# Kernel tuning notes

Measured on AMD Instinct MI355X. Metric: run time of the kernel, lower is better.

Reference implementation:

```python
import jax, jax.numpy as jnp
import numpy as np

B, N, DIM, T, H, DH = 4, 2048, 512, 16, 8, 64
EPS = 1e-5


def setup_inputs() -> dict:
    key = jax.random.key(0)
    ks = jax.random.split(key, 7)
    x = jax.random.normal(ks[0], (B, N, DIM), dtype=jnp.float32)
    # time-distance matrix, e.g. months between scans, in [0, 24)
    R = jax.random.uniform(ks[1], (B, T, T), dtype=jnp.float32) * 24.0
    gamma = jnp.ones((DIM,), dtype=jnp.float32)
    beta = jnp.zeros((DIM,), dtype=jnp.float32)
    W_qkv = jax.random.normal(ks[2], (DIM, 3 * H * DH), dtype=jnp.float32) * 0.02
    W_out = jax.random.normal(ks[3], (H * DH, DIM), dtype=jnp.float32) * 0.02
    a = jax.random.uniform(ks[4], (H,), dtype=jnp.float32)          # torch.rand(heads)
    c = 12.0 * jax.random.uniform(ks[5], (H,), dtype=jnp.float32)   # 12 * torch.rand(heads)
    return {"x": x, "R": R, "gamma": gamma, "beta": beta,
            "W_qkv": W_qkv, "W_out": W_out, "a": a, "c": c}


def reference(x, R, gamma, beta, W_qkv, W_out, a, c):
    b, n, dim = x.shape
    t = R.shape[-1]
    num_patches = n // t
    scale = DH ** -0.5

    # LayerNorm
    mu = jnp.mean(x, axis=-1, keepdims=True)
    var = jnp.mean(jnp.square(x - mu), axis=-1, keepdims=True)
    xn = (x - mu) * jax.lax.rsqrt(var + EPS) * gamma + beta

    # QKV projection -> [b, h, n, d]
    qkv = xn @ W_qkv  # [b, n, 3*h*d]
    q, k, v = jnp.split(qkv, 3, axis=-1)
    def to_heads(z):
        return z.reshape(b, n, H, DH).transpose(0, 2, 1, 3)
    q, k, v = to_heads(q), to_heads(k), to_heads(v)

    # attention scores with ReLU then learned sigmoid time-decay mask
    dots = jnp.einsum('bhnd,bhmd->bhnm', q, k) * scale
    dots = jax.nn.relu(dots)

    # flipped-sigmoid decay: 1 / (1 + exp(|a|*R - |c|)), per head  -> [b, h, t, t]
    decay = 1.0 / (1.0 + jnp.exp(jnp.abs(a)[None, :, None, None] * R[:, None, :, :]
                                 - jnp.abs(c)[None, :, None, None]))
    # expand timepoint mask to token resolution (repeat_interleave on both axes)
    decay = jnp.repeat(jnp.repeat(decay, num_patches, axis=2), num_patches, axis=3)

    attn = jax.nn.softmax(dots * decay, axis=-1)
    out = jnp.einsum('bhnm,bhmd->bhnd', attn, v)
    out = out.transpose(0, 2, 1, 3).reshape(b, n, H * DH)
    return out @ W_out  # dropout is identity at eval
```

## Files before the change

kernel.cpp:

```cpp
#include <hip/hip_runtime.h>
#include <math.h>

#define B_   4
#define N_   2048
#define DIM_ 512
#define T_   16
#define H_   8
#define DH_  64

typedef unsigned short ushort_t;
typedef __attribute__((ext_vector_type(8))) short bf16x8;
typedef __attribute__((ext_vector_type(16))) float f32x16;

__device__ inline ushort_t bf16_rn(float x) {
  unsigned u = __builtin_bit_cast(unsigned, x);
  u += 0x7FFFu + ((u >> 16) & 1u);
  return (ushort_t)(u >> 16);
}
__device__ inline float bf16f(ushort_t h) {
  return __builtin_bit_cast(float, (unsigned)h << 16);
}
__device__ inline unsigned pack2(ushort_t a, ushort_t b) {
  return (unsigned)a | ((unsigned)b << 16);
}
__device__ inline void split2(float x, ushort_t &h, ushort_t &l) {
  h = bf16_rn(x);
  l = bf16_rn(x - bf16f(h));
}

__global__ __launch_bounds__(256) void prep_kernel(
    const float* __restrict__ x, const float* __restrict__ gamma,
    const float* __restrict__ beta, const float* __restrict__ Wqkv,
    const float* __restrict__ Wout,
    ushort_t* __restrict__ xnh, ushort_t* __restrict__ xnl,
    ushort_t* __restrict__ wqh, ushort_t* __restrict__ wql,
    ushort_t* __restrict__ woh, ushort_t* __restrict__ wol) {
  __shared__ float Ts[64][68];
  int bidx = blockIdx.x;
  int tid = threadIdx.x;
  if (bidx < 256) {
    const float* src; ushort_t* dh; ushort_t* dl; int Nn, n0, k0;
    if (bidx < 192) {
      src = Wqkv; dh = wqh; dl = wql; Nn = 1536;
      n0 = (bidx % 24) * 64; k0 = (bidx / 24) * 64;
    } else {
      int l = bidx - 192;
      src = Wout; dh = woh; dl = wol; Nn = 512;
      n0 = (l % 8) * 64; k0 = (l / 8) * 64;
    }
#pragma unroll
    for (int it = 0; it < 4; ++it) {
      int idx = tid + it * 256;
      int r = idx >> 4, c4 = (idx & 15) * 4;
      *(float4*)&Ts[r][c4] = *(const float4*)&src[(size_t)(k0 + r) * Nn + n0 + c4];
    }
    __syncthreads();
#pragma unroll
    for (int it = 0; it < 2; ++it) {
      int idx = tid + it * 256;
      int n = idx >> 3, kc = (idx & 7) * 8;
      ushort_t hs[8], ls[8];
#pragma unroll
      for (int j = 0; j < 8; ++j) split2(Ts[kc + j][n], hs[j], ls[j]);
      uint4 uh, ul;
      uh.x = pack2(hs[0], hs[1]); uh.y = pack2(hs[2], hs[3]);
      uh.z = pack2(hs[4], hs[5]); uh.w = pack2(hs[6], hs[7]);
      ul.x = pack2(ls[0], ls[1]); ul.y = pack2(ls[2], ls[3]);
      ul.z = pack2(ls[4], ls[5]); ul.w = pack2(ls[6], ls[7]);
      size_t o = (size_t)(n0 + n) * 512 + k0 + kc;
      *(uint4*)&dh[o] = uh;
      *(uint4*)&dl[o] = ul;
    }
  } else {
    int row  = (bidx - 256) * 4 + (tid >> 6);
    int lane = tid & 63;
    const float4* xr = (const float4*)(x + (size_t)row * DIM_);
    float4 v0 = xr[lane * 2 + 0];
    float4 v1 = xr[lane * 2 + 1];
    float s  = v0.x + v0.y + v0.z + v0.w + v1.x + v1.y + v1.z + v1.w;
    float ss = v0.x*v0.x + v0.y*v0.y + v0.z*v0.z + v0.w*v0.w
             + v1.x*v1.x + v1.y*v1.y + v1.z*v1.z + v1.w*v1.w;
#pragma unroll
    for (int off = 32; off > 0; off >>= 1) {
      s  += __shfl_xor(s, off);
      ss += __shfl_xor(ss, off);
    }
    float mu  = s * (1.0f / DIM_);
    float var = ss * (1.0f / DIM_) - mu * mu;
    float rstd = rsqrtf(var + 1e-5f);
    float4 g0 = *(const float4*)&gamma[lane * 8];
    float4 g1 = *(const float4*)&gamma[lane * 8 + 4];
    float4 b0 = *(const float4*)&beta[lane * 8];
    float4 b1 = *(const float4*)&beta[lane * 8 + 4];
    float xv[8] = {v0.x, v0.y, v0.z, v0.w, v1.x, v1.y, v1.z, v1.w};
    float gv[8] = {g0.x, g0.y, g0.z, g0.w, g1.x, g1.y, g1.z, g1.w};
    float bv[8] = {b0.x, b0.y, b0.z, b0.w, b1.x, b1.y, b1.z, b1.w};
    ushort_t hs[8], ls[8];
#pragma unroll
    for (int j = 0; j < 8; ++j) {
      float xn = (xv[j] - mu) * rstd * gv[j] + bv[j];
      split2(xn, hs[j], ls[j]);
    }
    uint4 uh, ul;
    uh.x = pack2(hs[0], hs[1]); uh.y = pack2(hs[2], hs[3]);
    uh.z = pack2(hs[4], hs[5]); uh.w = pack2(hs[6], hs[7]);
    ul.x = pack2(ls[0], ls[1]); ul.y = pack2(ls[2], ls[3]);
    ul.z = pack2(ls[4], ls[5]); ul.w = pack2(ls[6], ls[7]);
    size_t o = (size_t)row * DIM_ + lane * 8;
    *(uint4*)&xnh[o] = uh;
    *(uint4*)&xnl[o] = ul;
  }
}

__global__ __launch_bounds__(256) void qkv_gemm_mfma(
    const ushort_t* __restrict__ xnh, const ushort_t* __restrict__ xnl,
    const ushort_t* __restrict__ wth, const ushort_t* __restrict__ wtl,
    ushort_t* __restrict__ qh, ushort_t* __restrict__ ql,
    ushort_t* __restrict__ kho, ushort_t* __restrict__ klo,
    ushort_t* __restrict__ vt) {
  __shared__ ushort_t Ah[128 * 40], Al[128 * 40], Bh[128 * 40], Bl[128 * 40];
  int tid = threadIdx.x;
  int w = tid >> 6, lane = tid & 63, l31 = lane & 31, g = lane >> 5;
  int wm = w >> 1, wn = w & 1;
  int idx = blockIdx.x;
  int xcd = idx & 7, local = idx >> 3;
  int n0 = (local % 12) * 128;
  int m0 = ((local / 12) * 8 + xcd) * 128;

  f32x16 acc[2][2];
#pragma unroll
  for (int i = 0; i < 2; ++i)
#pragma unroll
    for (int j = 0; j < 2; ++j)
#pragma unroll
      for (int e = 0; e < 16; ++e) acc[i][j][e] = 0.0f;

  int fm[2], fc[2];
#pragma unroll
  for (int it = 0; it < 2; ++it) {
    int f = tid + it * 256;
    fm[it] = f >> 2;
    fc[it] = (f & 3) * 8;
  }

#pragma unroll 1
  for (int kt = 0; kt < 16; ++kt) {
    __syncthreads();
#pragma unroll
    for (int it = 0; it < 2; ++it) {
      size_t ao = (size_t)(m0 + fm[it]) * 512 + kt * 32 + fc[it];
      size_t bo = (size_t)(n0 + fm[it]) * 512 + kt * 32 + fc[it];
      uint4 tah = *(const uint4*)&xnh[ao];
      uint4 tal = *(const uint4*)&xnl[ao];
      uint4 tbh = *(const uint4*)&wth[bo];
      uint4 tbl = *(const uint4*)&wtl[bo];
      int o = fm[it] * 40 + fc[it];
      *(uint4*)&Ah[o] = tah;
      *(uint4*)&Al[o] = tal;
      *(uint4*)&Bh[o] = tbh;
      *(uint4*)&Bl[o] = tbl;
    }
    __syncthreads();
#pragma unroll
    for (int kc = 0; kc < 2; ++kc) {
      int off = kc * 16 + 8 * g;
      bf16x8 afh[2], afl[2], bfh[2], bfl[2];
#pragma unroll
      for (int rb = 0; rb < 2; ++rb) {
        int r = (wm * 64 + rb * 32 + l31) * 40 + off;
        afh[rb] = *(const bf16x8*)&Ah[r];
        afl[rb] = *(const bf16x8*)&Al[r];
      }
#pragma unroll
      for (int cb = 0; cb < 2; ++cb) {
        int r = (wn * 64 + cb * 32 + l31) * 40 + off;
        bfh[cb] = *(const bf16x8*)&Bh[r];
        bfl[cb] = *(const bf16x8*)&Bl[r];
      }
#pragma unroll
      for (int rb = 0; rb < 2; ++rb)
#pragma unroll
        for (int cb = 0; cb < 2; ++cb) {
          acc[rb][cb] = __builtin_amdgcn_mfma_f32_32x32x16_bf16(afh[rb], bfh[cb], acc[rb][cb], 0, 0, 0);
          acc[rb][cb] = __builtin_amdgcn_mfma_f32_32x32x16_bf16(afh[rb], bfl[cb], acc[rb][cb], 0, 0, 0);
          acc[rb][cb] = __builtin_amdgcn_mfma_f32_32x32x16_bf16(afl[rb], bfh[cb], acc[rb][cb], 0, 0, 0);
        }
    }
  }

  int part = n0 >> 9;
#pragma unroll
  for (int rb = 0; rb < 2; ++rb) {
    int m_base = m0 + wm * 64 + rb * 32;
#pragma unroll
    for (int cb = 0; cb < 2; ++cb) {
      int n_g = n0 + wn * 64 + cb * 32 + l31;
      int rem = n_g & 511, hh = rem >> 6, d = rem & 63;
      if (part == 2) {
#pragma unroll
        for (int grp = 0; grp < 4; ++grp) {
          int m_g = m_base + grp * 8 + 4 * g;
          int bb = m_g >> 11, tok = m_g & 2047;
          uint2 pk;
          pk.x = pack2(bf16_rn(acc[rb][cb][grp * 4 + 0]), bf16_rn(acc[rb][cb][grp * 4 + 1]));
          pk.y = pack2(bf16_rn(acc[rb][cb][grp * 4 + 2]), bf16_rn(acc[rb][cb][grp * 4 + 3]));
          *(uint2*)&vt[((size_t)(bb * 8 + hh) * 64 + d) * 2048 + tok] = pk;
        }
      } else {
        float sc = (part == 0) ? 0.125f : 1.0f;
        ushort_t* dsth = (part == 0) ? qh : kho;
        ushort_t* dstl = (part == 0) ? ql : klo;
#pragma unroll
        for (int reg = 0; reg < 16; ++reg) {
          int row = (reg & 3) + 8 * (reg >> 2) + 4 * g;
          int m_g = m_base + row;
          int bb = m_g >> 11, tok = m_g & 2047;
          ushort_t hi, lo;
          split2(acc[rb][cb][reg] * sc, hi, lo);
          size_t addr = ((size_t)(bb * 8 + hh) * 2048 + tok) * 64 + d;
          dsth[addr] = hi;
          dstl[addr] = lo;
        }
      }
    }
  }
}

__global__ __launch_bounds__(512) void attn_mfma(
    const ushort_t* __restrict__ qh, const ushort_t* __restrict__ ql,
    const ushort_t* __restrict__ kho, const ushort_t* __restrict__ klo,
    const ushort_t* __restrict__ vt, const float* __restrict__ R,
    const float* __restrict__ a, const float* __restrict__ c,
    ushort_t* __restrict__ aoh, ushort_t* __restrict__ aol) {
  __shared__ ushort_t KhS[64 * 72], KlS[64 * 72], VtS[64 * 72];
  __shared__ ushort_t PS[256 * 72];

  int tid = threadIdx.x;
  int w = tid >> 6, lane = tid & 63, l31 = lane & 31, g = lane >> 5;
  int bh = blockIdx.x;
  int qt = blockIdx.y;
  int b = bh >> 3, h = bh & 7;
  float aab = fabsf(a[h]);
  float cab = fabsf(c[h]);

  int qrow = qt * 256 + w * 32 + l31;
  size_t qoff = ((size_t)bh * 2048 + qrow) * 64;
  bf16x8 qfh[4], qfl[4];
#pragma unroll
  for (int d0i = 0; d0i < 4; ++d0i) {
    qfh[d0i] = *(const bf16x8*)&qh[qoff + d0i * 16 + 8 * g];
    qfl[d0i] = *(const bf16x8*)&ql[qoff + d0i * 16 + 8 * g];
  }

  int frow = tid >> 3;
  int fcc = (tid & 7) * 8;
  const ushort_t* kbase = kho + (size_t)bh * 2048 * 64;
  const ushort_t* lbase = klo + (size_t)bh * 2048 * 64;
  const ushort_t* vbase = vt + (size_t)bh * 64 * 2048;

  f32x16 oacc[2];
#pragma unroll
  for (int t = 0; t < 2; ++t)
#pragma unroll
    for (int i = 0; i < 16; ++i) oacc[t][i] = 0.0f;
  float rs_acc[16] = {};
  int ti = qt * 2 + (w >> 2);

#pragma unroll 1
  for (int kt = 0; kt < 32; ++kt) {
    __syncthreads();
    {
      uint4 tk = *(const uint4*)&kbase[(size_t)(kt * 64 + frow) * 64 + fcc];
      uint4 tl = *(const uint4*)&lbase[(size_t)(kt * 64 + frow) * 64 + fcc];
      uint4 tv = *(const uint4*)&vbase[(size_t)frow * 2048 + kt * 64 + fcc];
      int o = frow * 72 + fcc;
      *(uint4*)&KhS[o] = tk;
      *(uint4*)&KlS[o] = tl;
      *(uint4*)&VtS[o] = tv;
    }
    __syncthreads();

    float Rv = R[b * (T_ * T_) + ti * T_ + (kt >> 1)];
    float dec = 1.0f / (1.0f + __expf(aab * Rv - cab));

#pragma unroll
    for (int khalf = 0; khalf < 2; ++khalf) {
      f32x16 sacc;
#pragma unroll
      for (int i = 0; i < 16; ++i) sacc[i] = 0.0f;
      int krow = (khalf * 32 + l31) * 72;
#pragma unroll
      for (int d0i = 0; d0i < 4; ++d0i) {
        int off = krow + d0i * 16 + 8 * g;
        bf16x8 kfh = *(const bf16x8*)&KhS[off];
        bf16x8 kfl = *(const bf16x8*)&KlS[off];
        sacc = __builtin_amdgcn_mfma_f32_32x32x16_bf16(qfh[d0i], kfh, sacc, 0, 0, 0);
        sacc = __builtin_amdgcn_mfma_f32_32x32x16_bf16(qfh[d0i], kfl, sacc, 0, 0, 0);
        sacc = __builtin_amdgcn_mfma_f32_32x32x16_bf16(qfl[d0i], kfh, sacc, 0, 0, 0);
      }
#pragma unroll
      for (int reg = 0; reg < 16; ++reg) {
        float pv = __expf(fmaxf(sacc[reg], 0.0f) * dec);
        rs_acc[reg] += pv;
        int row = (reg & 3) + 8 * (reg >> 2) + 4 * g;
        PS[(w * 32 + row) * 72 + khalf * 32 + l31] = bf16_rn(pv);
      }
    }

    bf16x8 pf[4];
#pragma unroll
    for (int k0i = 0; k0i < 4; ++k0i)
      pf[k0i] = *(const bf16x8*)&PS[(w * 32 + l31) * 72 + k0i * 16 + 8 * g];
#pragma unroll
    for (int dt = 0; dt < 2; ++dt) {
      int vrow = (dt * 32 + l31) * 72;
#pragma unroll
      for (int k0i = 0; k0i < 4; ++k0i) {
        bf16x8 vf = *(const bf16x8*)&VtS[vrow + k0i * 16 + 8 * g];
        oacc[dt] = __builtin_amdgcn_mfma_f32_32x32x16_bf16(pf[k0i], vf, oacc[dt], 0, 0, 0);
      }
    }
  }

#pragma unroll
  for (int reg = 0; reg < 16; ++reg) {
    float vsum = rs_acc[reg];
    vsum += __shfl_xor(vsum, 1);
    vsum += __shfl_xor(vsum, 2);
    vsum += __shfl_xor(vsum, 4);
    vsum += __shfl_xor(vsum, 8);
    vsum += __shfl_xor(vsum, 16);
    rs_acc[reg] = vsum;
  }

#pragma unroll
  for (int reg = 0; reg < 16; ++reg) {
    int row = (reg & 3) + 8 * (reg >> 2) + 4 * g;
    float invs = 1.0f / rs_acc[reg];
    int tok = qt * 256 + w * 32 + row;
#pragma unroll
    for (int dt = 0; dt < 2; ++dt) {
      int d = dt * 32 + l31;
      ushort_t hi, lo;
      split2(oacc[dt][reg] * invs, hi, lo);
      size_t addr = ((size_t)b * 2048 + tok) * 512 + h * 64 + d;
      aoh[addr] = hi;
      aol[addr] = lo;
    }
  }
}

__global__ __launch_bounds__(256) void out_gemm_mfma(
    const ushort_t* __restrict__ ah, const ushort_t* __restrict__ al,
    const ushort_t* __restrict__ wth, const ushort_t* __restrict__ wtl,
    float* __restrict__ out) {
  __shared__ ushort_t Ah[128 * 40], Al[128 * 40], Bh[128 * 40], Bl[128 * 40];
  int tid = threadIdx.x;
  int w = tid >> 6, lane = tid & 63, l31 = lane & 31, g = lane >> 5;
  int wm = w >> 1, wn = w & 1;
  int idx = blockIdx.x;
  int xcd = idx & 7, local = idx >> 3;
  int n0 = (local & 3) * 128;
  int m0 = ((local >> 2) * 8 + xcd) * 128;

  f32x16 acc[2][2];
#pragma unroll
  for (int i = 0; i < 2; ++i)
#pragma unroll
    for (int j = 0; j < 2; ++j)
#pragma unroll
      for (int e = 0; e < 16; ++e) acc[i][j][e] = 0.0f;

  int fm[2], fc[2];
#pragma unroll
  for (int it = 0; it < 2; ++it) {
    int f = tid + it * 256;
    fm[it] = f >> 2;
    fc[it] = (f & 3) * 8;
  }

#pragma unroll 1
  for (int kt = 0; kt < 16; ++kt) {
    __syncthreads();
#pragma unroll
    for (int it = 0; it < 2; ++it) {
      size_t ao = (size_t)(m0 + fm[it]) * 512 + kt * 32 + fc[it];
      size_t bo = (size_t)(n0 + fm[it]) * 512 + kt * 32 + fc[it];
      uint4 tah = *(const uint4*)&ah[ao];
      uint4 tal = *(const uint4*)&al[ao];
      uint4 tbh = *(const uint4*)&wth[bo];
      uint4 tbl = *(const uint4*)&wtl[bo];
      int o = fm[it] * 40 + fc[it];
      *(uint4*)&Ah[o] = tah;
      *(uint4*)&Al[o] = tal;
      *(uint4*)&Bh[o] = tbh;
      *(uint4*)&Bl[o] = tbl;
    }
    __syncthreads();
#pragma unroll
    for (int kc = 0; kc < 2; ++kc) {
      int off = kc * 16 + 8 * g;
      bf16x8 afh[2], afl[2], bfh[2], bfl[2];
#pragma unroll
      for (int rb = 0; rb < 2; ++rb) {
        int r = (wm * 64 + rb * 32 + l31) * 40 + off;
        afh[rb] = *(const bf16x8*)&Ah[r];
        afl[rb] = *(const bf16x8*)&Al[r];
      }
#pragma unroll
      for (int cb = 0; cb < 2; ++cb) {
        int r = (wn * 64 + cb * 32 + l31) * 40 + off;
        bfh[cb] = *(const bf16x8*)&Bh[r];
        bfl[cb] = *(const bf16x8*)&Bl[r];
      }
#pragma unroll
      for (int rb = 0; rb < 2; ++rb)
#pragma unroll
        for (int cb = 0; cb < 2; ++cb) {
          acc[rb][cb] = __builtin_amdgcn_mfma_f32_32x32x16_bf16(afh[rb], bfh[cb], acc[rb][cb], 0, 0, 0);
          acc[rb][cb] = __builtin_amdgcn_mfma_f32_32x32x16_bf16(afh[rb], bfl[cb], acc[rb][cb], 0, 0, 0);
          acc[rb][cb] = __builtin_amdgcn_mfma_f32_32x32x16_bf16(afl[rb], bfh[cb], acc[rb][cb], 0, 0, 0);
        }
    }
  }

#pragma unroll
  for (int rb = 0; rb < 2; ++rb) {
    int m_base = m0 + wm * 64 + rb * 32;
#pragma unroll
    for (int cb = 0; cb < 2; ++cb) {
      int n_g = n0 + wn * 64 + cb * 32 + l31;
#pragma unroll
      for (int reg = 0; reg < 16; ++reg) {
        int row = (reg & 3) + 8 * (reg >> 2) + 4 * g;
        out[(size_t)(m_base + row) * 512 + n_g] = acc[rb][cb][reg];
      }
    }
  }
}

extern "C" void kernel_launch(void* const* d_in, const int* in_sizes, int n_in,
                              void* d_out, int out_size, void* d_ws, size_t ws_size,
                              hipStream_t stream) {
  (void)in_sizes; (void)n_in;
  const float* x     = (const float*)d_in[0];
  const float* R     = (const float*)d_in[1];
  const float* gamma = (const float*)d_in[2];
  const float* beta  = (const float*)d_in[3];
  const float* Wqkv  = (const float*)d_in[4];
  const float* Wout  = (const float*)d_in[5];
  const float* av    = (const float*)d_in[6];
  const float* cv    = (const float*)d_in[7];
  float* out = (float*)d_out;

  const size_t EL  = (size_t)B_ * N_ * DIM_;
  const size_t SZT = EL * sizeof(ushort_t);

  char* p = (char*)d_ws;
  ushort_t* wqh = (ushort_t*)p;                  p += (size_t)1536 * 512 * 2;
  ushort_t* wql = (ushort_t*)p;                  p += (size_t)1536 * 512 * 2;
  ushort_t* woh = (ushort_t*)p;                  p += (size_t)512 * 512 * 2;
  ushort_t* wol = (ushort_t*)p;                  p += (size_t)512 * 512 * 2;
  ushort_t* qhb = (ushort_t*)p;                  p += SZT;
  ushort_t* qlb = (ushort_t*)p;                  p += SZT;
  ushort_t* khb = (ushort_t*)p;                  p += SZT;
  ushort_t* klb = (ushort_t*)p;                  p += SZT;
  ushort_t* vtb = (ushort_t*)p;                  p += SZT;
  size_t base_need = (size_t)(p - (char*)d_ws);
  size_t needA = base_need + 2 * SZT;

  bool planA = (ws_size >= needA);
  ushort_t* xnh = planA ? (ushort_t*)p : (ushort_t*)d_out;
  ushort_t* xnl = xnh + EL;
  float* gemm_dst = planA ? out : (float*)qhb;

  prep_kernel<<<dim3(2304), dim3(256), 0, stream>>>(x, gamma, beta, Wqkv, Wout,
                                                    xnh, xnl, wqh, wql, woh, wol);
  qkv_gemm_mfma<<<dim3(768), dim3(256), 0, stream>>>(xnh, xnl, wqh, wql,
                                                     qhb, qlb, khb, klb, vtb);
  attn_mfma<<<dim3(32, 8), dim3(512), 0, stream>>>(qhb, qlb, khb, klb, vtb,
                                                   R, av, cv, xnh, xnl);
  out_gemm_mfma<<<dim3(256), dim3(256), 0, stream>>>(xnh, xnl, woh, wol, gemm_dst);
  if (!planA) {
    hipMemcpyAsync(out, gemm_dst, (size_t)out_size * sizeof(float),
                   hipMemcpyDeviceToDevice, stream);
  }
}
```

Before: 244.9 us.

## Keep attention probabilities in registers via transposed S and permlane swap

The attention kernel now computes S transposed (K as the A operand), so each lane holds one query's scores. The probabilities are packed to bf16 with v_cvt_pk_bf16_f32 and rearranged with v_permlane32_swap into the A-operand layout for the PV MFMA, which removes the shared-memory P round trip. Row sums become a per-lane scalar instead of a 5-step shuffle reduction, and exp is rewritten as exp2 with log2e folded into the decay. The block shrinks to 4 waves covering 128 query rows, with twice as many blocks, so each block reloads K/V tiles for fewer queries and global traffic rises.

Result: no change. 240.4 us (-1.8%).

```diff
diff --git a/kernel.cpp b/kernel.cpp
--- a/kernel.cpp
+++ b/kernel.cpp
@@ -26,6 +26,14 @@
 __device__ inline void split2(float x, ushort_t &h, ushort_t &l) {
   h = bf16_rn(x);
   l = bf16_rn(x - bf16f(h));
+}
+__device__ inline unsigned cvt_pk_bf16(float lo, float hi) {
+  unsigned r;
+  asm("v_cvt_pk_bf16_f32 %0, %1, %2" : "=v"(r) : "v"(lo), "v"(hi));
+  return r;
+}
+__device__ inline void permlane32_swap(unsigned &x, unsigned &y) {
+  asm volatile("v_permlane32_swap_b32 %0, %1" : "+v"(x), "+v"(y));
 }
 
 __global__ __launch_bounds__(256) void prep_kernel(
@@ -226,14 +234,14 @@
   }
 }
 
-__global__ __launch_bounds__(512) void attn_mfma(
+__global__ __launch_bounds__(256) void attn_mfma(
     const ushort_t* __restrict__ qh, const ushort_t* __restrict__ ql,
     const ushort_t* __restrict__ kho, const ushort_t* __restrict__ klo,
     const ushort_t* __restrict__ vt, const float* __restrict__ R,
     const float* __restrict__ a, const float* __restrict__ c,
     ushort_t* __restrict__ aoh, ushort_t* __restrict__ aol) {
   __shared__ ushort_t KhS[64 * 72], KlS[64 * 72], VtS[64 * 72];
-  __shared__ ushort_t PS[256 * 72];
+  __shared__ float rsS[128];
 
   int tid = threadIdx.x;
   int w = tid >> 6, lane = tid & 63, l31 = lane & 31, g = lane >> 5;
@@ -243,7 +251,7 @@
   float aab = fabsf(a[h]);
   float cab = fabsf(c[h]);
 
-  int qrow = qt * 256 + w * 32 + l31;
+  int qrow = qt * 128 + w * 32 + l31;
   size_t qoff = ((size_t)bh * 2048 + qrow) * 64;
   bf16x8 qfh[4], qfl[4];
 #pragma unroll
@@ -252,8 +260,6 @@
     qfl[d0i] = *(const bf16x8*)&ql[qoff + d0i * 16 + 8 * g];
   }
 
-  int frow = tid >> 3;
-  int fcc = (tid & 7) * 8;
   const ushort_t* kbase = kho + (size_t)bh * 2048 * 64;
   const ushort_t* lbase = klo + (size_t)bh * 2048 * 64;
   const ushort_t* vbase = vt + (size_t)bh * 64 * 2048;
@@ -263,26 +269,35 @@
   for (int t = 0; t < 2; ++t)
 #pragma unroll
     for (int i = 0; i < 16; ++i) oacc[t][i] = 0.0f;
-  float rs_acc[16] = {};
-  int ti = qt * 2 + (w >> 2);
+  float rs = 0.0f;
+
+  int frow[2], fcc[2];
+#pragma unroll
+  for (int it = 0; it < 2; ++it) {
+    int idx = tid + it * 256;
+    frow[it] = idx >> 3;
+    fcc[it] = (idx & 7) * 8;
+  }
 
 #pragma unroll 1
   for (int kt = 0; kt < 32; ++kt) {
     __syncthreads();
-    {
-      uint4 tk = *(const uint4*)&kbase[(size_t)(kt * 64 + frow) * 64 + fcc];
-      uint4 tl = *(const uint4*)&lbase[(size_t)(kt * 64 + frow) * 64 + fcc];
-      uint4 tv = *(const uint4*)&vbase[(size_t)frow * 2048 + kt * 64 + fcc];
-      int o = frow * 72 + fcc;
+#pragma unroll
+    for (int it = 0; it < 2; ++it) {
+      uint4 tk = *(const uint4*)&kbase[(size_t)(kt * 64 + frow[it]) * 64 + fcc[it]];
+      uint4 tl = *(const uint4*)&lbase[(size_t)(kt * 64 + frow[it]) * 64 + fcc[it]];
+      uint4 tv = *(const uint4*)&vbase[(size_t)frow[it] * 2048 + kt * 64 + fcc[it]];
+      int o = frow[it] * 72 + fcc[it];
       *(uint4*)&KhS[o] = tk;
       *(uint4*)&KlS[o] = tl;
       *(uint4*)&VtS[o] = tv;
     }
     __syncthreads();
 
-    float Rv = R[b * (T_ * T_) + ti * T_ + (kt >> 1)];
-    float dec = 1.0f / (1.0f + __expf(aab * Rv - cab));
-
+    float Rv = R[b * (T_ * T_) + qt * T_ + (kt >> 1)];
+    float decl2 = 1.4426950408889634f / (1.0f + __expf(aab * Rv - cab));
+
+    bf16x8 pa[4];
 #pragma unroll
     for (int khalf = 0; khalf < 2; ++khalf) {
       f32x16 sacc;
@@ -294,50 +309,48 @@
         int off = krow + d0i * 16 + 8 * g;
         bf16x8 kfh = *(const bf16x8*)&KhS[off];
         bf16x8 kfl = *(const bf16x8*)&KlS[off];
-        sacc = __builtin_amdgcn_mfma_f32_32x32x16_bf16(qfh[d0i], kfh, sacc, 0, 0, 0);
-        sacc = __builtin_amdgcn_mfma_f32_32x32x16_bf16(qfh[d0i], kfl, sacc, 0, 0, 0);
-        sacc = __builtin_amdgcn_mfma_f32_32x32x16_bf16(qfl[d0i], kfh, sacc, 0, 0, 0);
+        sacc = __builtin_amdgcn_mfma_f32_32x32x16_bf16(kfh, qfh[d0i], sacc, 0, 0, 0);
+        sacc = __builtin_amdgcn_mfma_f32_32x32x16_bf16(kfl, qfh[d0i], sacc, 0, 0, 0);
+        sacc = __builtin_amdgcn_mfma_f32_32x32x16_bf16(kfh, qfl[d0i], sacc, 0, 0, 0);
       }
 #pragma unroll
       for (int reg = 0; reg < 16; ++reg) {
-        float pv = __expf(fmaxf(sacc[reg], 0.0f) * dec);
-        rs_acc[reg] += pv;
-        int row = (reg & 3) + 8 * (reg >> 2) + 4 * g;
-        PS[(w * 32 + row) * 72 + khalf * 32 + l31] = bf16_rn(pv);
-      }
-    }
-
-    bf16x8 pf[4];
-#pragma unroll
-    for (int k0i = 0; k0i < 4; ++k0i)
-      pf[k0i] = *(const bf16x8*)&PS[(w * 32 + l31) * 72 + k0i * 16 + 8 * g];
+        float pv = exp2f(fmaxf(sacc[reg], 0.0f) * decl2);
+        rs += pv;
+        sacc[reg] = pv;
+      }
+#pragma unroll
+      for (int hf = 0; hf < 2; ++hf) {
+        unsigned d0 = cvt_pk_bf16(sacc[hf * 8 + 0], sacc[hf * 8 + 1]);
+        unsigned d1 = cvt_pk_bf16(sacc[hf * 8 + 2], sacc[hf * 8 + 3]);
+        unsigned d2 = cvt_pk_bf16(sacc[hf * 8 + 4], sacc[hf * 8 + 5]);
+        unsigned d3 = cvt_pk_bf16(sacc[hf * 8 + 6], sacc[hf * 8 + 7]);
+        permlane32_swap(d0, d2);
+        permlane32_swap(d1, d3);
+        uint4 u; u.x = d0; u.y = d1; u.z = d2; u.w = d3;
+        pa[khalf * 2 + hf] = __builtin_bit_cast(bf16x8, u);
+      }
+    }
+
 #pragma unroll
     for (int dt = 0; dt < 2; ++dt) {
       int vrow = (dt * 32 + l31) * 72;
 #pragma unroll
-      for (int k0i = 0; k0i < 4; ++k0i) {
-        bf16x8 vf = *(const bf16x8*)&VtS[vrow + k0i * 16 + 8 * g];
-        oacc[dt] = __builtin_amdgcn_mfma_f32_32x32x16_bf16(pf[k0i], vf, oacc[dt], 0, 0, 0);
-      }
-    }
-  }
-
-#pragma unroll
-  for (int reg = 0; reg < 16; ++reg) {
-    float vsum = rs_acc[reg];
-    vsum += __shfl_xor(vsum, 1);
-    vsum += __shfl_xor(vsum, 2);
-    vsum += __shfl_xor(vsum, 4);
-    vsum += __shfl_xor(vsum, 8);
-    vsum += __shfl_xor(vsum, 16);
-    rs_acc[reg] = vsum;
-  }
+      for (int kc = 0; kc < 4; ++kc) {
+        bf16x8 vf = *(const bf16x8*)&VtS[vrow + kc * 16 + 8 * g];
+        oacc[dt] = __builtin_amdgcn_mfma_f32_32x32x16_bf16(pa[kc], vf, oacc[dt], 0, 0, 0);
+      }
+    }
+  }
+
+  rs += __shfl_xor(rs, 32);
+  rsS[w * 32 + l31] = rs;
 
 #pragma unroll
   for (int reg = 0; reg < 16; ++reg) {
     int row = (reg & 3) + 8 * (reg >> 2) + 4 * g;
-    float invs = 1.0f / rs_acc[reg];
-    int tok = qt * 256 + w * 32 + row;
+    float invs = 1.0f / rsS[w * 32 + row];
+    int tok = qt * 128 + w * 32 + row;
 #pragma unroll
     for (int dt = 0; dt < 2; ++dt) {
       int d = dt * 32 + l31;
@@ -478,8 +491,8 @@
                                                     xnh, xnl, wqh, wql, woh, wol);
   qkv_gemm_mfma<<<dim3(768), dim3(256), 0, stream>>>(xnh, xnl, wqh, wql,
                                                      qhb, qlb, khb, klb, vtb);
-  attn_mfma<<<dim3(32, 8), dim3(512), 0, stream>>>(qhb, qlb, khb, klb, vtb,
-                                                   R, av, cv, xnh, xnl);
+  attn_mfma<<<dim3(32, 16), dim3(256), 0, stream>>>(qhb, qlb, khb, klb, vtb,
+                                                    R, av, cv, xnh, xnl);
   out_gemm_mfma<<<dim3(256), dim3(256), 0, stream>>>(xnh, xnl, woh, wol, gemm_dst);
   if (!planA) {
     hipMemcpyAsync(out, gemm_dst, (size_t)out_size * sizeof(float),
```
